# Kernel tuning notes

Hardware: AMD Instinct MI355X
Metric: run time of the kernel (lower is better)

The kernel has to match this reference:

```python
import jax, jax.numpy as jnp
import numpy as np

B_, N_, D_ = 8, 1024, 64
H_, DH_ = 4, 16
DI_, DS_, DTR_ = 128, 64, 4
MAXP = 512


def _ln(x, w, b, eps=1e-5):
    m = jnp.mean(x, -1, keepdims=True)
    v = jnp.mean((x - m) ** 2, -1, keepdims=True)
    return (x - m) * jax.lax.rsqrt(v + eps) * w + b


def _attn(x, drop_mask, Wq, Wkv, Wo, bo, rel_emb):
    b, n, d = x.shape
    scale = DH_ ** -0.5
    q = (x @ Wq).reshape(b, n, H_, DH_).transpose(0, 2, 1, 3)
    kv = x @ Wkv
    k = kv[..., :d].reshape(b, n, H_, DH_).transpose(0, 2, 1, 3)
    v = kv[..., d:].reshape(b, n, H_, DH_).transpose(0, 2, 1, 3)
    dots = jnp.einsum('bhid,bhjd->bhij', q, k) * scale
    seq = jnp.arange(n)
    dist = jnp.clip(seq[:, None] - seq[None, :], -MAXP, MAXP) + MAXP
    rpe = rel_emb[dist]  # (n, n, DH_)
    dots = dots + jnp.einsum('bhid,ijd->bhij', q, rpe) * scale
    # stochastic key drop: Bernoulli(0.3) positions get -1e12
    dots = dots + drop_mask.astype(dots.dtype) * (-1e12)
    attn = jax.nn.softmax(dots, axis=-1)
    out = jnp.einsum('bhij,bhjd->bhid', attn, v)
    out = out.transpose(0, 2, 1, 3).reshape(b, n, H_ * DH_)
    return out @ Wo + bo


def _mamba(x, W_in, conv_w, conv_b, W_xproj, W_dt, b_dt, A_log, Dm, W_out):
    b, n, _ = x.shape
    xz = x @ W_in                      # (b, n, 2*DI_)
    u, z = xz[..., :DI_], xz[..., DI_:]
    uc = u.transpose(0, 2, 1)          # (b, DI_, n)
    uc = jax.lax.conv_general_dilated(
        uc, conv_w[:, None, :], (1,), ((3, 0),),
        feature_group_count=DI_, dimension_numbers=('NCH', 'OIH', 'NCH'))
    uc = uc + conv_b[None, :, None]
    u = jax.nn.silu(uc).transpose(0, 2, 1)  # (b, n, DI_)
    xdb = u @ W_xproj                  # (b, n, DTR_+2*DS_)
    dt = jax.nn.softplus(xdb[..., :DTR_] @ W_dt + b_dt)  # (b, n, DI_)
    Bm = xdb[..., DTR_:DTR_ + DS_]
    Cm = xdb[..., DTR_ + DS_:]
    A = -jnp.exp(A_log)                # (DI_, DS_)

    def step(h, inp):
        dt_t, B_t, C_t, u_t = inp      # (b,DI_),(b,DS_),(b,DS_),(b,DI_)
        dA = jnp.exp(dt_t[..., None] * A)
        h = h * dA + (dt_t * u_t)[..., None] * B_t[:, None, :]
        y = jnp.einsum('bds,bs->bd', h, C_t)
        return h, y

    h0 = jnp.zeros((b, DI_, DS_), x.dtype)
    xs = (dt.transpose(1, 0, 2), Bm.transpose(1, 0, 2),
          Cm.transpose(1, 0, 2), u.transpose(1, 0, 2))
    _, ys = jax.lax.scan(step, h0, xs)
    y = ys.transpose(1, 0, 2) + u * Dm
    y = y * jax.nn.silu(z)
    return y @ W_out


def _rmsgn(x, gamma, eps=1e-5, groups=4):
    shp = x.shape
    dpg = shp[-1] // groups
    xg = x.reshape(shp[:-1] + (groups, dpg))
    rms = jnp.sqrt(jnp.sum(xg * xg, -1, keepdims=True)) * (dpg ** -0.5)
    return (xg / (rms + eps)).reshape(shp) * gamma


def _ff1(x, c1_w, c1_b, d1_w, d1_b):
    # SwiGLUConvDeconv1d(64, 256, kernel=4, shift=1); x: (b, s2, 64)
    s2 = x.shape[1]
    xc = x.transpose(0, 2, 1)
    xc = jnp.pad(xc, ((0, 0), (0, 0), (3, 3)))
    xc = jax.lax.conv_general_dilated(
        xc, c1_w, (1,), 'VALID', dimension_numbers=('NCH', 'OIH', 'NCH'))
    xc = xc + c1_b[None, :, None]
    gate = jax.nn.silu(xc[:, 256:, :])
    xc = xc[:, :256, :] * gate
    # ConvTranspose1d stride 1 == conv with flipped kernel, full padding
    w = jnp.flip(d1_w, -1).transpose(1, 0, 2)  # (64, 256, 4)
    xc = jax.lax.conv_general_dilated(
        xc, w, (1,), ((3, 3),), dimension_numbers=('NCH', 'OIH', 'NCH'))
    xc = xc + d1_b[None, :, None]
    out = xc.transpose(0, 2, 1)
    return out[:, 3:3 + s2, :]


def _forward(x, drop_mask, ln1_w, ln1_b, Wq, Wkv, Wo, bo, rel_emb,
             ln2_w, ln2_b, W_in, conv_w, conv_b, W_xproj, W_dt, b_dt,
             A_log, Dm, W_out, gamma, c1_w, c1_b, d1_w, d1_b, ln3_w, ln3_b):
    xt = _ln(x, ln1_w, ln1_b)
    xt = _attn(xt, drop_mask, Wq, Wkv, Wo, bo, rel_emb) + x
    x = x + xt  # dropout p=0 -> identity (faithful to original residual math)
    xt = _ln(x, ln2_w, ln2_b)
    m = _mamba(xt, W_in, conv_w, conv_b, W_xproj, W_dt, b_dt, A_log, Dm, W_out)
    m = jnp.where(m >= 0, m, 0.01 * m)  # leaky_relu
    m = _rmsgn(m, gamma)
    m = m + 0.5 * _ff1(m, c1_w, c1_b, d1_w, d1_b)
    x = x + m
    return _ln(x, ln3_w, ln3_b)


def setup_inputs() -> dict:
    ks = jax.random.split(jax.random.key(0), 16)
    g = lambda i, shp, s: jax.random.normal(ks[i], shp, dtype=jnp.float32) * s
    A_log = jnp.log(jnp.tile(jnp.arange(1, DS_ + 1, dtype=jnp.float32)[None, :], (DI_, 1)))
    return {
        'x': jax.random.normal(ks[0], (B_, N_, D_), dtype=jnp.float32),
        'drop_mask': jax.random.bernoulli(ks[1], 0.3, (B_, H_, N_, N_)),
        'ln1_w': jnp.ones((D_,), jnp.float32), 'ln1_b': jnp.zeros((D_,), jnp.float32),
        'Wq': g(2, (D_, D_), 0.1), 'Wkv': g(3, (D_, 2 * D_), 0.1),
        'Wo': g(4, (D_, D_), 0.1), 'bo': jnp.zeros((D_,), jnp.float32),
        'rel_emb': g(5, (2 * MAXP + 1, DH_), 0.02),
        'ln2_w': jnp.ones((D_,), jnp.float32), 'ln2_b': jnp.zeros((D_,), jnp.float32),
        'W_in': g(6, (D_, 2 * DI_), 0.1),
        'conv_w': g(7, (DI_, 4), 0.2), 'conv_b': jnp.zeros((DI_,), jnp.float32),
        'W_xproj': g(8, (DI_, DTR_ + 2 * DS_), 0.1),
        'W_dt': g(9, (DTR_, DI_), 0.1), 'b_dt': jnp.zeros((DI_,), jnp.float32),
        'A_log': A_log, 'Dm': jnp.ones((DI_,), jnp.float32),
        'W_out': g(10, (DI_, D_), 0.1),
        'gamma': jnp.ones((D_,), jnp.float32),
        'c1_w': g(11, (512, 64, 4), 0.1), 'c1_b': jnp.zeros((512,), jnp.float32),
        'd1_w': g(12, (256, 64, 4), 0.1), 'd1_b': jnp.zeros((64,), jnp.float32),
        'ln3_w': jnp.ones((D_,), jnp.float32), 'ln3_b': jnp.zeros((D_,), jnp.float32),
    }


def reference(x, drop_mask, ln1_w, ln1_b, Wq, Wkv, Wo, bo, rel_emb,
              ln2_w, ln2_b, W_in, conv_w, conv_b, W_xproj, W_dt, b_dt,
              A_log, Dm, W_out, gamma, c1_w, c1_b, d1_w, d1_b, ln3_w, ln3_b):
    return _forward(x, drop_mask, ln1_w, ln1_b, Wq, Wkv, Wo, bo, rel_emb,
                    ln2_w, ln2_b, W_in, conv_w, conv_b, W_xproj, W_dt, b_dt,
                    A_log, Dm, W_out, gamma, c1_w, c1_b, d1_w, d1_b, ln3_w, ln3_b)
```

## Files before the change

### kernel.cpp

```cpp
#include <hip/hip_runtime.h>
#include <math.h>


__device__ __forceinline__ float wsum64(float v){
#pragma unroll
  for(int m=32;m>0;m>>=1) v += __shfl_xor(v, m, 64);
  return v;
}
__device__ __forceinline__ float wmax64(float v){
#pragma unroll
  for(int m=32;m>0;m>>=1) v = fmaxf(v, __shfl_xor(v, m, 64));
  return v;
}
__device__ __forceinline__ float silu_f(float x){ return x / (1.f + __expf(-x)); }
__device__ __forceinline__ int clip512(int d){ return d < -512 ? -512 : (d > 512 ? 512 : d); }

__global__ __launch_bounds__(256) void k_relT(
    const float* __restrict__ rel, float* __restrict__ relT){
  int idx = blockIdx.x*256 + threadIdx.x;
  if (idx < 16*1025){
    int c = idx / 1025;
    int d = idx - c*1025;
    relT[idx] = rel[d*16 + c];
  }
}

__global__ __launch_bounds__(256) void k_c1wT(
    const float* __restrict__ c1w, float* __restrict__ c1wT){
  int idx = blockIdx.x*256 + threadIdx.x;
  int row = idx >> 9;
  int i   = idx & 511;
  c1wT[idx] = c1w[(size_t)i*256 + row];
}

__global__ __launch_bounds__(256) void k_ln1_qkv(
    const float* __restrict__ x, const float* __restrict__ w1, const float* __restrict__ b1,
    const float* __restrict__ Wq, const float* __restrict__ Wkv,
    float* __restrict__ qb, float* __restrict__ kbT, float* __restrict__ vbT){
  int lane = threadIdx.x & 63, warp = threadIdx.x >> 6;
  int token = blockIdx.x*4 + warp;
  __shared__ float xt[4][64];
  float xv = x[(size_t)token*64 + lane];
  float mean = wsum64(xv) * 0.015625f;
  float dlt = xv - mean;
  float var = wsum64(dlt*dlt) * 0.015625f;
  float xn = dlt * rsqrtf(var + 1e-5f) * w1[lane] + b1[lane];
  xt[warp][lane] = xn;
  __syncthreads();
  float aq=0.f, ak=0.f, av=0.f;
#pragma unroll 4
  for(int dd=0; dd<64; ++dd){
    float xd = xt[warp][dd];
    aq += xd * Wq[dd*64 + lane];
    ak += xd * Wkv[dd*128 + lane];
    av += xd * Wkv[dd*128 + 64 + lane];
  }
  int b = token >> 10, i = token & 1023;
  int h = lane >> 4, dh = lane & 15;
  size_t o  = (((size_t)(b*4 + h))*1024 + i)*16 + dh;
  size_t oT = (((size_t)(b*4 + h))*16 + dh)*1024 + i;
  qb[o]=aq; kbT[oT]=ak; vbT[oT]=av;
}

__global__ __launch_bounds__(256, 4) void k_attn(
    const float* __restrict__ qb, const float* __restrict__ kbT, const float* __restrict__ vbT,
    const int* __restrict__ dmask, const float* __restrict__ relT,
    float* __restrict__ attn_raw){
  int tid = threadIdx.x;
  int lane = tid & 63, wv = tid >> 6;
  int bh  = blockIdx.y;
  int i0  = blockIdx.x*8;
  int b = bh >> 2, h = bh & 3;
  int r0 = wv*2, r1 = wv*2 + 1;
  int i_a = i0 + r0, i_b = i0 + r1;

  __shared__ float qs[8][16];
  __shared__ float relS[16][80];
  __shared__ float Gc[8][64];
  __shared__ float red[8][16][17];
  __shared__ float sums[8];

  if (tid < 128){
    int r = tid >> 4, c = tid & 15;
    qs[r][c] = qb[((size_t)bh*1024 + i0 + r)*16 + c] * 0.25f;
  }
  __syncthreads();
  float q0[16], q1[16];
#pragma unroll
  for(int c=0;c<16;++c){ q0[c]=qs[r0][c]; q1[c]=qs[r1][c]; }

  const float* kb = kbT + (size_t)bh*16*1024;
  const float* vb = vbT + (size_t)bh*16*1024;
  const int* mb0 = dmask + ((size_t)bh*1024 + i_a)*1024;
  const int* mb1 = dmask + ((size_t)bh*1024 + i_b)*1024;

  float m0=-3.0e38f, m1=-3.0e38f, s0=0.f, s1=0.f;
  float a0[16], a1[16];
#pragma unroll
  for(int c=0;c<16;++c){ a0[c]=0.f; a1[c]=0.f; }

#pragma unroll 1
  for(int t=0;t<16;++t){
    int j0 = 64*t;
    int dlo = clip512(i0 - j0 - 63) + 512;
#pragma unroll
    for(int e0=0;e0<5;++e0){
      int e = tid + 256*e0;
      int c = e / 80, dd = e - c*80;
      int d = dlo + dd; d = d > 1024 ? 1024 : d;
      relS[c][dd] = relT[c*1025 + d];
    }
    __syncthreads();
#pragma unroll
    for(int p=0;p<2;++p){
      int e = tid + 256*p;
      int r = e >> 6, jj = e & 63;
      int dd = clip512(i0 + r - j0 - jj) + 512 - dlo;
      float g = 0.f;
#pragma unroll
      for(int c=0;c<16;++c) g += qs[r][c]*relS[c][dd];
      Gc[r][jj] = g;
    }
    __syncthreads();
    int j = j0 + lane;
    float kk[16];
#pragma unroll
    for(int c=0;c<16;++c) kk[c] = kb[c*1024 + j];
    float sv0 = Gc[r0][lane] + (mb0[j] ? -1.0e12f : 0.0f);
    float sv1 = Gc[r1][lane] + (mb1[j] ? -1.0e12f : 0.0f);
#pragma unroll
    for(int c=0;c<16;++c){ sv0 += q0[c]*kk[c]; sv1 += q1[c]*kk[c]; }
    float vv[16];
#pragma unroll
    for(int c=0;c<16;++c) vv[c] = vb[c*1024 + j];
    float mn0 = fmaxf(m0, sv0);
    float al0 = __expf(m0 - mn0);
    float p0  = __expf(sv0 - mn0);
    m0 = mn0; s0 = s0*al0 + p0;
#pragma unroll
    for(int c=0;c<16;++c) a0[c] = a0[c]*al0 + p0*vv[c];
    float mn1 = fmaxf(m1, sv1);
    float al1 = __expf(m1 - mn1);
    float p1  = __expf(sv1 - mn1);
    m1 = mn1; s1 = s1*al1 + p1;
#pragma unroll
    for(int c=0;c<16;++c) a1[c] = a1[c]*al1 + p1*vv[c];
  }
  float M0 = wmax64(m0), M1 = wmax64(m1);
  float sc0 = __expf(m0 - M0), sc1 = __expf(m1 - M1);
  s0 = wsum64(s0*sc0); s1 = wsum64(s1*sc1);
#pragma unroll
  for(int c=0;c<16;++c){
    float x0 = a0[c]*sc0;
    x0 += __shfl_xor(x0, 32, 64); x0 += __shfl_xor(x0, 16, 64);
    a0[c] = x0;
    float x1 = a1[c]*sc1;
    x1 += __shfl_xor(x1, 32, 64); x1 += __shfl_xor(x1, 16, 64);
    a1[c] = x1;
  }
  __syncthreads();
  if (lane < 16){
#pragma unroll
    for(int c=0;c<16;++c){ red[r0][lane][c] = a0[c]; red[r1][lane][c] = a1[c]; }
  }
  if (lane == 0){ sums[r0] = s0; sums[r1] = s1; }
  __syncthreads();
  if (tid < 128){
    int row = tid >> 4, c = tid & 15;
    float tot = 0.f;
#pragma unroll
    for(int g=0; g<16; ++g) tot += red[row][g][c];
    int irow = i0 + row;
    attn_raw[((size_t)b*1024 + irow)*64 + h*16 + c] = tot / sums[row];
  }
}

__global__ __launch_bounds__(256) void k_post_attn(
    const float* __restrict__ x, const float* __restrict__ attn_raw,
    const float* __restrict__ Wo, const float* __restrict__ bo,
    const float* __restrict__ ln2w, const float* __restrict__ ln2b,
    const float* __restrict__ W_in,
    float* __restrict__ x2, float* __restrict__ u0, float* __restrict__ zsarr){
  int lane = threadIdx.x & 63, warp = threadIdx.x >> 6;
  int token = blockIdx.x*4 + warp;
  __shared__ float ar[4][64];
  __shared__ float lnv[4][64];
  ar[warp][lane] = attn_raw[(size_t)token*64 + lane];
  __syncthreads();
  float acc = bo[lane];
#pragma unroll 4
  for(int dd=0;dd<64;++dd) acc += ar[warp][dd]*Wo[dd*64+lane];
  float t = 2.f*x[(size_t)token*64+lane] + acc;
  x2[(size_t)token*64+lane] = t;
  float mean = wsum64(t)*0.015625f;
  float dlt = t-mean;
  float var = wsum64(dlt*dlt)*0.015625f;
  float ln = dlt*rsqrtf(var+1e-5f)*ln2w[lane]+ln2b[lane];
  lnv[warp][lane]=ln;
  __syncthreads();
  float a0=0.f,a1=0.f,a2=0.f,a3=0.f;
#pragma unroll 4
  for(int dd=0;dd<64;++dd){
    float xd = lnv[warp][dd];
    const float* wr = W_in + dd*256;
    a0 += xd*wr[lane]; a1 += xd*wr[lane+64]; a2 += xd*wr[lane+128]; a3 += xd*wr[lane+192];
  }
  u0[(size_t)token*128 + lane] = a0;
  u0[(size_t)token*128 + 64 + lane] = a1;
  zsarr[(size_t)token*128 + lane] = silu_f(a2);
  zsarr[(size_t)token*128 + 64 + lane] = silu_f(a3);
}

__global__ __launch_bounds__(256) void k_conv_proj(
    const float* __restrict__ u0, const float* __restrict__ conv_w, const float* __restrict__ conv_b,
    const float* __restrict__ W_xproj, const float* __restrict__ W_dt, const float* __restrict__ b_dt,
    float* __restrict__ uarr, float* __restrict__ Bmp, float* __restrict__ Cmp, float* __restrict__ dtarr){
  int sub = threadIdx.x >> 7, c = threadIdx.x & 127;
  int token = blockIdx.x*2 + sub;
  int b = token >> 10, i = token & 1023;
  __shared__ float us[2][128];
  __shared__ float dtin[2][4];
  float acc = conv_b[c];
#pragma unroll
  for(int k2=0;k2<4;++k2){
    int t2 = i - 3 + k2;
    if (t2 >= 0) acc += u0[((size_t)b*1024 + t2)*128 + c]*conv_w[c*4+k2];
  }
  float uv = silu_f(acc);
  uarr[(size_t)token*128 + c] = uv;
  us[sub][c] = uv;
  __syncthreads();
  float accA = 0.f, accB = 0.f;
  int cB = 128 + (c & 3);
#pragma unroll 4
  for(int dd=0; dd<128; ++dd){
    float xd = us[sub][dd];
    accA += xd * W_xproj[dd*132 + c];
    accB += xd * W_xproj[dd*132 + cB];
  }
  if (c < 4){ dtin[sub][c] = accA; Cmp[(size_t)token*64 + 60 + c] = accB; }
  else if (c < 68) Bmp[(size_t)token*64 + (c-4)] = accA;
  else             Cmp[(size_t)token*64 + (c-68)] = accA;
  __syncthreads();
  float dv = b_dt[c];
#pragma unroll
  for(int r2=0;r2<4;++r2) dv += dtin[sub][r2]*W_dt[r2*128 + c];
  dv = fmaxf(dv, 0.f) + log1pf(expf(-fabsf(dv)));
  dtarr[(size_t)token*128 + c] = dv;
}

__global__ __launch_bounds__(256) void k_scan(
    const float* __restrict__ dtarr, const float* __restrict__ uarr,
    const float* __restrict__ Bmp, const float* __restrict__ Cmp,
    const float* __restrict__ zsarr, const float* __restrict__ A_log,
    const float* __restrict__ Dm, float* __restrict__ ymp){
  int lane = threadIdx.x & 63, warp = threadIdx.x >> 6;
  int g = blockIdx.x*4 + warp;
  int b = g >> 7, d = g & 127;
  float A = -expf(A_log[d*64 + lane]);
  float Dv = Dm[d];
  const float* dtp = dtarr + (size_t)b*1024*128 + d;
  const float* up  = uarr  + (size_t)b*1024*128 + d;
  const float* zp  = zsarr + (size_t)b*1024*128 + d;
  const float* Bp  = Bmp   + (size_t)b*1024*64 + lane;
  const float* Cp  = Cmp   + (size_t)b*1024*64 + lane;
  float* yp        = ymp   + (size_t)b*1024*128 + d;
  float h = 0.f;
  for(int t0=0; t0<1024; t0+=8){
    float dtc[8], uc[8], Bc[8], Cc[8], zc[8];
#pragma unroll
    for(int r=0;r<8;++r){
      dtc[r]=dtp[(size_t)(t0+r)*128]; uc[r]=up[(size_t)(t0+r)*128];
      Bc[r]=Bp[(size_t)(t0+r)*64];    Cc[r]=Cp[(size_t)(t0+r)*64];
      zc[r]=zp[(size_t)(t0+r)*128];
    }
    float hc[8];
#pragma unroll
    for(int r=0;r<8;++r){
      float dt = dtc[r];
      h = h*__expf(dt*A) + dt*uc[r]*Bc[r];
      hc[r] = h*Cc[r];
    }
    float y[8];
#pragma unroll
    for(int r=0;r<8;++r) y[r] = wsum64(hc[r]);
    if (lane==0){
#pragma unroll
      for(int r=0;r<8;++r) yp[(size_t)(t0+r)*128] = (y[r] + uc[r]*Dv)*zc[r];
    }
  }
}

__global__ __launch_bounds__(256) void k_wout(
    const float* __restrict__ ymp, const float* __restrict__ W_out,
    const float* __restrict__ gamma, float* __restrict__ marr){
  int lane = threadIdx.x & 63, warp = threadIdx.x >> 6;
  int token = blockIdx.x*4 + warp;
  __shared__ float ys[4][128];
  ys[warp][lane]      = ymp[(size_t)token*128 + lane];
  ys[warp][lane+64]   = ymp[(size_t)token*128 + 64 + lane];
  __syncthreads();
  float acc = 0.f;
#pragma unroll 4
  for(int dd=0; dd<128; ++dd) acc += ys[warp][dd]*W_out[dd*64 + lane];
  acc = acc >= 0.f ? acc : 0.01f*acc;
  float ss = acc*acc;
#pragma unroll
  for(int m=1;m<16;m<<=1) ss += __shfl_xor(ss, m, 64);
  float rms = sqrtf(ss)*0.25f;
  marr[(size_t)token*64 + lane] = acc/(rms + 1e-5f)*gamma[lane];
}

__global__ __launch_bounds__(256) void k_h2(
    const float* __restrict__ marr, const float* __restrict__ c1wT,
    const float* __restrict__ c1b, float* __restrict__ h2){
  int b = blockIdx.y;
  int t0 = blockIdx.x * 16;
  int tid = threadIdx.x;
  __shared__ float ms[19][64];
  for(int l = tid; l < 19*64; l += 256){
    int row = l >> 6, cc = l & 63;
    int t = t0 - 3 + row;
    ms[row][cc] = (t >= 0 && t < 1024) ? marr[((size_t)b*1024 + t)*64 + cc] : 0.f;
  }
  __syncthreads();
  int i = tid;
  float acc1[16], acc2[16];
#pragma unroll
  for(int tl=0;tl<16;++tl){ acc1[tl]=0.f; acc2[tl]=0.f; }
  for(int cc=0; cc<64; ++cc){
    float mv[19];
#pragma unroll
    for(int r2=0;r2<19;++r2) mv[r2] = ms[r2][cc];
    const float* wr = c1wT + (size_t)cc*4*512;
    float wa0 = wr[      i], wa1 = wr[ 512+i], wa2 = wr[1024+i], wa3 = wr[1536+i];
    float wg0 = wr[  256+i], wg1 = wr[ 768+i], wg2 = wr[1280+i], wg3 = wr[1792+i];
#pragma unroll
    for(int tl=0; tl<16; ++tl){
      acc1[tl] += wa0*mv[tl+0] + wa1*mv[tl+1] + wa2*mv[tl+2] + wa3*mv[tl+3];
      acc2[tl] += wg0*mv[tl+0] + wg1*mv[tl+1] + wg2*mv[tl+2] + wg3*mv[tl+3];
    }
  }
  float bb1 = c1b[i], bb2 = c1b[i+256];
#pragma unroll
  for(int tl=0; tl<16; ++tl){
    int t = t0 + tl;
    if (t < 1027){
      float o1 = acc1[tl] + bb1;
      float o2 = acc2[tl] + bb2;
      h2[((size_t)b*1027 + t)*256 + i] = o1 * silu_f(o2);
    }
  }
}

__global__ __launch_bounds__(256) void k_ff_final(
    const float* __restrict__ h2, const float* __restrict__ d1w, const float* __restrict__ d1b,
    const float* __restrict__ x2, const float* __restrict__ marr,
    const float* __restrict__ ln3w, const float* __restrict__ ln3b,
    float* __restrict__ out){
  int b = blockIdx.y;
  int s0 = blockIdx.x * 16;
  int tid = threadIdx.x;
  int o = tid & 63, sg = tid >> 6;
  __shared__ float hs[19][256];
  for(int l = tid; l < 19*256; l += 256){
    int row = l >> 8, cc = l & 255;
    hs[row][cc] = h2[((size_t)b*1027 + s0 + row)*256 + cc];
  }
  __syncthreads();
  int sl = sg*4;
  float acc0=0.f, acc1=0.f, acc2=0.f, acc3=0.f;
  const float4* wb = (const float4*)d1w + o;
#pragma unroll 2
  for(int i2=0; i2<256; ++i2){
    float4 wv = wb[(size_t)i2*64];
    float h0=hs[sl+0][i2], h1=hs[sl+1][i2], h2v=hs[sl+2][i2], h3=hs[sl+3][i2];
    float h4=hs[sl+4][i2], h5=hs[sl+5][i2], h6=hs[sl+6][i2];
    acc0 += h0*wv.w + h1*wv.z + h2v*wv.y + h3*wv.x;
    acc1 += h1*wv.w + h2v*wv.z + h3*wv.y + h4*wv.x;
    acc2 += h2v*wv.w + h3*wv.z + h4*wv.y + h5*wv.x;
    acc3 += h3*wv.w + h4*wv.z + h5*wv.y + h6*wv.x;
  }
  float accs[4] = {acc0, acc1, acc2, acc3};
  float bo_ = d1b[o];
#pragma unroll
  for(int r=0;r<4;++r){
    int s = s0 + sl + r;
    size_t idx = ((size_t)b*1024 + s)*64 + o;
    float tot = x2[idx] + marr[idx] + 0.5f*(accs[r] + bo_);
    float mean = wsum64(tot)*0.015625f;
    float dlt = tot - mean;
    float var = wsum64(dlt*dlt)*0.015625f;
    out[idx] = dlt*rsqrtf(var+1e-5f)*ln3w[o] + ln3b[o];
  }
}

extern "C" void kernel_launch(void* const* d_in, const int* in_sizes, int n_in,
                              void* d_out, int out_size, void* d_ws, size_t ws_size,
                              hipStream_t stream){
  const float* x       = (const float*)d_in[0];
  const int*   dmask   = (const int*)  d_in[1];
  const float* ln1w    = (const float*)d_in[2];
  const float* ln1b    = (const float*)d_in[3];
  const float* Wq      = (const float*)d_in[4];
  const float* Wkv     = (const float*)d_in[5];
  const float* Wo      = (const float*)d_in[6];
  const float* bo      = (const float*)d_in[7];
  const float* rel     = (const float*)d_in[8];
  const float* ln2w    = (const float*)d_in[9];
  const float* ln2b    = (const float*)d_in[10];
  const float* W_in    = (const float*)d_in[11];
  const float* conv_w  = (const float*)d_in[12];
  const float* conv_b  = (const float*)d_in[13];
  const float* W_xproj = (const float*)d_in[14];
  const float* W_dt    = (const float*)d_in[15];
  const float* b_dt    = (const float*)d_in[16];
  const float* A_log   = (const float*)d_in[17];
  const float* Dm      = (const float*)d_in[18];
  const float* W_out   = (const float*)d_in[19];
  const float* gamma   = (const float*)d_in[20];
  const float* c1w     = (const float*)d_in[21];
  const float* c1b     = (const float*)d_in[22];
  const float* d1w     = (const float*)d_in[23];
  const float* d1b     = (const float*)d_in[24];
  const float* ln3w    = (const float*)d_in[25];
  const float* ln3b    = (const float*)d_in[26];
  float* outp = (float*)d_out;

  float* ws = (float*)d_ws;
  float* qb       = ws;
  float* kbT      = qb      + 524288;
  float* vbT      = kbT     + 524288;
  float* attn_raw = vbT     + 524288;
  float* x2       = attn_raw+ 524288;
  float* u0       = x2      + 524288;
  float* zsarr    = u0      + 1048576;
  float* uarr     = zsarr   + 1048576;
  float* dtarr    = uarr    + 1048576;
  float* Bmp      = dtarr   + 1048576;
  float* Cmp      = Bmp     + 524288;
  float* ymp      = Cmp     + 524288;
  float* marr     = ymp     + 1048576;
  float* h2       = marr    + 524288;
  float* relT     = h2      + 2103296;
  float* c1wT     = relT    + 16400;

  k_relT     <<<65, 256, 0, stream>>>(rel, relT);
  k_c1wT     <<<512, 256, 0, stream>>>(c1w, c1wT);
  k_ln1_qkv  <<<2048, 256, 0, stream>>>(x, ln1w, ln1b, Wq, Wkv, qb, kbT, vbT);
  k_attn     <<<dim3(128,32), 256, 0, stream>>>(qb, kbT, vbT, dmask, relT, attn_raw);
  k_post_attn<<<2048, 256, 0, stream>>>(x, attn_raw, Wo, bo, ln2w, ln2b, W_in, x2, u0, zsarr);
  k_conv_proj<<<4096, 256, 0, stream>>>(u0, conv_w, conv_b, W_xproj, W_dt, b_dt, uarr, Bmp, Cmp, dtarr);
  k_scan     <<<256, 256, 0, stream>>>(dtarr, uarr, Bmp, Cmp, zsarr, A_log, Dm, ymp);
  k_wout     <<<2048, 256, 0, stream>>>(ymp, W_out, gamma, marr);
  k_h2       <<<dim3(65,8), 256, 0, stream>>>(marr, c1wT, c1b, h2);
  k_ff_final <<<dim3(64,8), 256, 0, stream>>>(h2, d1w, d1b, x2, marr, ln3w, ln3b, outp);
}
```

Measured before the change: 813.2 us.

## Precompute full rel-pos bias row, interleave K/V, fold weight transposes into QKV kernel

The attention kernel now computes the whole 8x1024 relative-position bias tile once up front, reading relT straight from global memory. This removes the per-tile shared-memory staging and the two block barriers inside each of the 16 iterations. K and V are stored interleaved as float2, so one load fetches both. The relT and c1w transpose kernels are folded into the LN1/QKV kernel's first blocks to save two launches. In exchange the kernel uses a larger 32KB shared buffer, so occupancy drops from 4 to 3 blocks per unit. The extra float2 register pressure is another risk.

```diff
diff --git a/kernel.cpp b/kernel.cpp
--- a/kernel.cpp
+++ b/kernel.cpp
@@ -14,29 +14,13 @@
 }
 __device__ __forceinline__ float silu_f(float x){ return x / (1.f + __expf(-x)); }
 __device__ __forceinline__ int clip512(int d){ return d < -512 ? -512 : (d > 512 ? 512 : d); }
-
-__global__ __launch_bounds__(256) void k_relT(
-    const float* __restrict__ rel, float* __restrict__ relT){
-  int idx = blockIdx.x*256 + threadIdx.x;
-  if (idx < 16*1025){
-    int c = idx / 1025;
-    int d = idx - c*1025;
-    relT[idx] = rel[d*16 + c];
-  }
-}
-
-__global__ __launch_bounds__(256) void k_c1wT(
-    const float* __restrict__ c1w, float* __restrict__ c1wT){
-  int idx = blockIdx.x*256 + threadIdx.x;
-  int row = idx >> 9;
-  int i   = idx & 511;
-  c1wT[idx] = c1w[(size_t)i*256 + row];
-}
 
 __global__ __launch_bounds__(256) void k_ln1_qkv(
     const float* __restrict__ x, const float* __restrict__ w1, const float* __restrict__ b1,
     const float* __restrict__ Wq, const float* __restrict__ Wkv,
-    float* __restrict__ qb, float* __restrict__ kbT, float* __restrict__ vbT){
+    const float* __restrict__ rel, const float* __restrict__ c1w,
+    float* __restrict__ qb, float2* __restrict__ kvT,
+    float* __restrict__ relT, float* __restrict__ c1wT){
   int lane = threadIdx.x & 63, warp = threadIdx.x >> 6;
   int token = blockIdx.x*4 + warp;
   __shared__ float xt[4][64];
@@ -59,11 +43,26 @@
   int h = lane >> 4, dh = lane & 15;
   size_t o  = (((size_t)(b*4 + h))*1024 + i)*16 + dh;
   size_t oT = (((size_t)(b*4 + h))*16 + dh)*1024 + i;
-  qb[o]=aq; kbT[oT]=ak; vbT[oT]=av;
-}
-
-__global__ __launch_bounds__(256, 4) void k_attn(
-    const float* __restrict__ qb, const float* __restrict__ kbT, const float* __restrict__ vbT,
+  qb[o]=aq;
+  kvT[oT] = make_float2(ak, av);
+
+  if (blockIdx.x < 65){
+    int idx = blockIdx.x*256 + threadIdx.x;
+    if (idx < 16*1025){
+      int c = idx / 1025;
+      int d = idx - c*1025;
+      relT[idx] = rel[d*16 + c];
+    }
+  } else if (blockIdx.x < 577){
+    int idx = (blockIdx.x-65)*256 + threadIdx.x;
+    int row = idx >> 9;
+    int ii  = idx & 511;
+    c1wT[idx] = c1w[(size_t)ii*256 + row];
+  }
+}
+
+__global__ __launch_bounds__(256, 3) void k_attn(
+    const float* __restrict__ qb, const float2* __restrict__ kvT,
     const int* __restrict__ dmask, const float* __restrict__ relT,
     float* __restrict__ attn_raw){
   int tid = threadIdx.x;
@@ -74,10 +73,8 @@
   int r0 = wv*2, r1 = wv*2 + 1;
   int i_a = i0 + r0, i_b = i0 + r1;
 
+  __shared__ float Gc[8][1024];
   __shared__ float qs[8][16];
-  __shared__ float relS[16][80];
-  __shared__ float Gc[8][64];
-  __shared__ float red[8][16][17];
   __shared__ float sums[8];
 
   if (tid < 128){
@@ -85,12 +82,25 @@
     qs[r][c] = qb[((size_t)bh*1024 + i0 + r)*16 + c] * 0.25f;
   }
   __syncthreads();
+
+  {
+    int r = tid >> 5, jb = tid & 31;
+#pragma unroll 1
+    for(int k=0;k<32;++k){
+      int j = jb + 32*k;
+      int d = clip512(i0 + r - j) + 512;
+      float g = 0.f;
+#pragma unroll
+      for(int c=0;c<16;++c) g += qs[r][c]*relT[c*1025 + d];
+      Gc[r][j] = g;
+    }
+  }
   float q0[16], q1[16];
 #pragma unroll
   for(int c=0;c<16;++c){ q0[c]=qs[r0][c]; q1[c]=qs[r1][c]; }
-
-  const float* kb = kbT + (size_t)bh*16*1024;
-  const float* vb = vbT + (size_t)bh*16*1024;
+  __syncthreads();
+
+  const float2* kvb = kvT + (size_t)bh*16*1024;
   const int* mb0 = dmask + ((size_t)bh*1024 + i_a)*1024;
   const int* mb1 = dmask + ((size_t)bh*1024 + i_b)*1024;
 
@@ -101,50 +111,27 @@
 
 #pragma unroll 1
   for(int t=0;t<16;++t){
-    int j0 = 64*t;
-    int dlo = clip512(i0 - j0 - 63) + 512;
-#pragma unroll
-    for(int e0=0;e0<5;++e0){
-      int e = tid + 256*e0;
-      int c = e / 80, dd = e - c*80;
-      int d = dlo + dd; d = d > 1024 ? 1024 : d;
-      relS[c][dd] = relT[c*1025 + d];
-    }
-    __syncthreads();
-#pragma unroll
-    for(int p=0;p<2;++p){
-      int e = tid + 256*p;
-      int r = e >> 6, jj = e & 63;
-      int dd = clip512(i0 + r - j0 - jj) + 512 - dlo;
-      float g = 0.f;
-#pragma unroll
-      for(int c=0;c<16;++c) g += qs[r][c]*relS[c][dd];
-      Gc[r][jj] = g;
-    }
-    __syncthreads();
-    int j = j0 + lane;
-    float kk[16];
-#pragma unroll
-    for(int c=0;c<16;++c) kk[c] = kb[c*1024 + j];
-    float sv0 = Gc[r0][lane] + (mb0[j] ? -1.0e12f : 0.0f);
-    float sv1 = Gc[r1][lane] + (mb1[j] ? -1.0e12f : 0.0f);
-#pragma unroll
-    for(int c=0;c<16;++c){ sv0 += q0[c]*kk[c]; sv1 += q1[c]*kk[c]; }
-    float vv[16];
-#pragma unroll
-    for(int c=0;c<16;++c) vv[c] = vb[c*1024 + j];
+    int j = lane + 64*t;
+    int mk0 = mb0[j], mk1 = mb1[j];
+    float2 kv[16];
+#pragma unroll
+    for(int c=0;c<16;++c) kv[c] = kvb[c*1024 + j];
+    float sv0 = Gc[r0][j] + (mk0 ? -1.0e12f : 0.0f);
+    float sv1 = Gc[r1][j] + (mk1 ? -1.0e12f : 0.0f);
+#pragma unroll
+    for(int c=0;c<16;++c){ sv0 += q0[c]*kv[c].x; sv1 += q1[c]*kv[c].x; }
     float mn0 = fmaxf(m0, sv0);
     float al0 = __expf(m0 - mn0);
     float p0  = __expf(sv0 - mn0);
     m0 = mn0; s0 = s0*al0 + p0;
 #pragma unroll
-    for(int c=0;c<16;++c) a0[c] = a0[c]*al0 + p0*vv[c];
+    for(int c=0;c<16;++c) a0[c] = a0[c]*al0 + p0*kv[c].y;
     float mn1 = fmaxf(m1, sv1);
     float al1 = __expf(m1 - mn1);
     float p1  = __expf(sv1 - mn1);
     m1 = mn1; s1 = s1*al1 + p1;
 #pragma unroll
-    for(int c=0;c<16;++c) a1[c] = a1[c]*al1 + p1*vv[c];
+    for(int c=0;c<16;++c) a1[c] = a1[c]*al1 + p1*kv[c].y;
   }
   float M0 = wmax64(m0), M1 = wmax64(m1);
   float sc0 = __expf(m0 - M0), sc1 = __expf(m1 - M1);
@@ -159,9 +146,13 @@
     a1[c] = x1;
   }
   __syncthreads();
+  float* red = &Gc[0][0];
   if (lane < 16){
 #pragma unroll
-    for(int c=0;c<16;++c){ red[r0][lane][c] = a0[c]; red[r1][lane][c] = a1[c]; }
+    for(int c=0;c<16;++c){
+      red[r0*272 + lane*17 + c] = a0[c];
+      red[r1*272 + lane*17 + c] = a1[c];
+    }
   }
   if (lane == 0){ sums[r0] = s0; sums[r1] = s1; }
   __syncthreads();
@@ -169,7 +160,7 @@
     int row = tid >> 4, c = tid & 15;
     float tot = 0.f;
 #pragma unroll
-    for(int g=0; g<16; ++g) tot += red[row][g][c];
+    for(int g=0; g<16; ++g) tot += red[row*272 + g*17 + c];
     int irow = i0 + row;
     attn_raw[((size_t)b*1024 + irow)*64 + h*16 + c] = tot / sums[row];
   }
@@ -429,9 +420,8 @@
 
   float* ws = (float*)d_ws;
   float* qb       = ws;
-  float* kbT      = qb      + 524288;
-  float* vbT      = kbT     + 524288;
-  float* attn_raw = vbT     + 524288;
+  float* kvT      = qb      + 524288;
+  float* attn_raw = kvT     + 1048576;
   float* x2       = attn_raw+ 524288;
   float* u0       = x2      + 524288;
   float* zsarr    = u0      + 1048576;
@@ -445,10 +435,9 @@
   float* relT     = h2      + 2103296;
   float* c1wT     = relT    + 16400;
 
-  k_relT     <<<65, 256, 0, stream>>>(rel, relT);
-  k_c1wT     <<<512, 256, 0, stream>>>(c1w, c1wT);
-  k_ln1_qkv  <<<2048, 256, 0, stream>>>(x, ln1w, ln1b, Wq, Wkv, qb, kbT, vbT);
-  k_attn     <<<dim3(128,32), 256, 0, stream>>>(qb, kbT, vbT, dmask, relT, attn_raw);
+  k_ln1_qkv  <<<2048, 256, 0, stream>>>(x, ln1w, ln1b, Wq, Wkv, rel, c1w,
+                                        qb, (float2*)kvT, relT, c1wT);
+  k_attn     <<<dim3(128,32), 256, 0, stream>>>(qb, (const float2*)kvT, dmask, relT, attn_raw);
   k_post_attn<<<2048, 256, 0, stream>>>(x, attn_raw, Wo, bo, ln2w, ln2b, W_in, x2, u0, zsarr);
   k_conv_proj<<<4096, 256, 0, stream>>>(u0, conv_w, conv_b, W_xproj, W_dt, b_dt, uarr, Bmp, Cmp, dtarr);
   k_scan     <<<256, 256, 0, stream>>>(dtarr, uarr, Bmp, Cmp, zsarr, A_log, Dm, ymp);
```

Measured after the change: 808.1 us. About the same (-0.6%).
